# Performance work log

Measured on AMD Instinct MI355X. Metric: run time of the kernel, lower is better.

## Reference

```python
import jax, jax.numpy as jnp
import numpy as np

NSAMPLE = 32
LAMBDA = 0.5


def setup_inputs() -> dict:
    key = jax.random.key(0)
    k1, k2, k3, k4, k5 = jax.random.split(key, 5)
    B, N, NPOINT, C, NCOMP = 4, 8192, 2048, 64, 16
    xyz = jax.random.normal(k1, (B, N, 3), dtype=jnp.float32)
    new_xyz = jax.random.normal(k2, (B, NPOINT, 3), dtype=jnp.float32)
    components = jax.random.randint(k3, (B, N, 1), 0, NCOMP, dtype=jnp.int64)
    new_components = jax.random.randint(k4, (B, NPOINT, 1), 0, NCOMP, dtype=jnp.int64)
    features = jax.random.normal(k5, (B, C, N), dtype=jnp.float32)
    return {"xyz": xyz, "new_xyz": new_xyz, "components": components,
            "new_components": new_components, "features": features}


def _gag_knn(new_xyz, xyz, new_comp, comp, k, lam):
    # squared pairwise distances (B, npoint, N), same math as sum((src-dst)**2)
    diff = new_xyz[:, :, None, :] - xyz[:, None, :, :]
    dists = jnp.sum(diff * diff, axis=-1)
    # component-aware rescale
    mask = comp[:, None, :] == new_comp[:, :, None]  # (B, npoint, N)
    dists = jnp.where(mask, dists * lam, dists * (1.0 - lam))
    # full argsort then take first k (faithful to original)
    idx = jnp.argsort(dists, axis=-1)[:, :, :k]  # (B, npoint, k)
    return idx.astype(jnp.int32)


def reference(xyz, new_xyz, components, new_components, features):
    comp = components[..., 0]
    new_comp = new_components[..., 0]
    idx = _gag_knn(new_xyz, xyz, new_comp, comp, NSAMPLE, LAMBDA)  # (B, npoint, ns)

    # group xyz: gather along N -> (B, npoint, ns, 3)
    grouped_xyz = jnp.take_along_axis(xyz[:, None, :, :], idx[..., None], axis=2)
    grouped_xyz = grouped_xyz - new_xyz[:, :, None, :]
    grouped_xyz = jnp.transpose(grouped_xyz, (0, 3, 1, 2))  # (B, 3, npoint, ns)

    # group features: (B, C, N) -> (B, npoint, ns, C) -> (B, C, npoint, ns)
    feats_bnc = jnp.transpose(features, (0, 2, 1))  # (B, N, C)
    grouped_feats = jnp.take_along_axis(feats_bnc[:, None, :, :], idx[..., None], axis=2)
    grouped_feats = jnp.transpose(grouped_feats, (0, 3, 1, 2))  # (B, C, npoint, ns)

    return jnp.concatenate([grouped_xyz, grouped_feats], axis=1)  # (B, 3+C, npoint, ns)
```

## Files before the change

### kernel.cpp

```cpp
#include <hip/hip_runtime.h>


#define BQ 4
#define NN_ 8192
#define NPOINT 2048
#define CF 64
#define NS 32
#define T1 256
#define PER (NN_ / T1)
#define CAP 1024

__global__ __launch_bounds__(256) void knn_kernel(const float* __restrict__ xyz,
                                                  const float* __restrict__ new_xyz,
                                                  int* __restrict__ idxOut) {
  const int q = blockIdx.x;
  const int b = q / NPOINT;
  const int tid = threadIdx.x;

  const float qx = new_xyz[q * 3 + 0];
  const float qy = new_xyz[q * 3 + 1];
  const float qz = new_xyz[q * 3 + 2];

  const float* __restrict__ base = xyz + (size_t)b * NN_ * 3;

  float d[PER];
  float lmin = 3.4e38f;
  int n = tid;
#pragma unroll
  for (int j = 0; j < PER; j++, n += T1) {
    float dx = base[n * 3 + 0] - qx;
    float dy = base[n * 3 + 1] - qy;
    float dz = base[n * 3 + 2] - qz;
    float dist = __fadd_rn(__fadd_rn(__fmul_rn(dx, dx), __fmul_rn(dy, dy)),
                           __fmul_rn(dz, dz));
    dist *= 0.5f;
    d[j] = dist;
    lmin = fminf(lmin, dist);
  }

  __shared__ float mins[T1];
  mins[tid] = lmin;
  __syncthreads();
  for (int k = 2; k <= T1; k <<= 1) {
    for (int j = k >> 1; j > 0; j >>= 1) {
      int ixj = tid ^ j;
      if (ixj > tid) {
        float a = mins[tid], bb = mins[ixj];
        bool up = ((tid & k) == 0);
        if (up ? (a > bb) : (a < bb)) { mins[tid] = bb; mins[ixj] = a; }
      }
      __syncthreads();
    }
  }
  const float theta = mins[NS - 1];

  __shared__ unsigned long long cand[CAP];
  __shared__ int cnt;
  if (tid == 0) cnt = 0;
  __syncthreads();
  n = tid;
#pragma unroll
  for (int j = 0; j < PER; j++, n += T1) {
    if (d[j] <= theta) {
      int pos = atomicAdd(&cnt, 1);
      if (pos < CAP)
        cand[pos] = ((unsigned long long)__float_as_uint(d[j]) << 32) | (unsigned)n;
    }
  }
  __syncthreads();
  int m = cnt < CAP ? cnt : CAP;

  for (int i = tid; i < m; i += T1) {
    unsigned long long x = cand[i];
    int r = 0;
    for (int j = 0; j < m; j++) r += (cand[j] < x) ? 1 : 0;
    if (r < NS) idxOut[q * NS + r] = (int)(x & 0xffffffffu);
  }
}

__global__ __launch_bounds__(256) void transpose_kernel(const float* __restrict__ f,
                                                        float* __restrict__ ft) {
  __shared__ float t[32][33];
  const int b = blockIdx.z;
  const int n0 = blockIdx.x * 32;
  const int c0 = blockIdx.y * 32;
  const int tx = threadIdx.x;
  const int ty = threadIdx.y;
#pragma unroll
  for (int i = 0; i < 4; i++) {
    int c = c0 + ty + i * 8;
    t[ty + i * 8][tx] = f[(size_t)b * CF * NN_ + (size_t)c * NN_ + n0 + tx];
  }
  __syncthreads();
#pragma unroll
  for (int i = 0; i < 4; i++) {
    int nrow = n0 + ty + i * 8;
    ft[(size_t)b * NN_ * CF + (size_t)nrow * CF + c0 + tx] = t[tx][ty + i * 8];
  }
}

#define FSTR 68
__global__ __launch_bounds__(256) void group_kernel(const float* __restrict__ xyz,
                                                    const float* __restrict__ new_xyz,
                                                    const float* __restrict__ featsT,
                                                    const int* __restrict__ idxArr,
                                                    float* __restrict__ out) {
  const int q = blockIdx.x;
  const int b = q / NPOINT;
  const int p = q - b * NPOINT;
  const int tid = threadIdx.x;

  __shared__ int sIdx[NS];
  __shared__ __align__(16) float ldsF[NS * FSTR];
  __shared__ float ldsX[3 * NS];

  if (tid < NS) sIdx[tid] = idxArr[q * NS + tid];
  __syncthreads();

  {
    int s = tid >> 3, r = tid & 7;
    int nn = sIdx[s];
    const float4* src = (const float4*)(featsT + ((size_t)b * NN_ + nn) * CF);
    float4 v0 = src[r * 2];
    float4 v1 = src[r * 2 + 1];
    float4* dst = (float4*)(ldsF + s * FSTR + r * 8);
    dst[0] = v0;
    dst[1] = v1;
  }
  if (tid < 96) {
    int dd = tid >> 5, s = tid & 31;
    int nn = sIdx[s];
    ldsX[dd * NS + s] = xyz[((size_t)b * NN_ + nn) * 3 + dd] -
                        new_xyz[(size_t)q * 3 + dd];
  }
  __syncthreads();

  const int s = tid & 31;
  const int r0 = tid >> 5;
#pragma unroll
  for (int k = 0; k < 9; k++) {
    int row = r0 + k * 8;
    if (row < 67) {
      float v = (row < 3) ? ldsX[row * NS + s] : ldsF[s * FSTR + (row - 3)];
      out[(((size_t)b * 67 + row) * NPOINT + p) * NS + s] = v;
    }
  }
}

extern "C" void kernel_launch(void* const* d_in, const int* in_sizes, int n_in,
                              void* d_out, int out_size, void* d_ws, size_t ws_size,
                              hipStream_t stream) {
  const float* xyz      = (const float*)d_in[0];
  const float* new_xyz  = (const float*)d_in[1];
  const float* features = (const float*)d_in[4];
  float* out = (float*)d_out;

  int* idxArr = (int*)d_ws;
  float* featsT = (float*)((char*)d_ws + (size_t)BQ * NPOINT * NS * sizeof(int));

  knn_kernel<<<BQ * NPOINT, T1, 0, stream>>>(xyz, new_xyz, idxArr);
  transpose_kernel<<<dim3(NN_ / 32, CF / 32, BQ), dim3(32, 8), 0, stream>>>(features, featsT);
  group_kernel<<<BQ * NPOINT, T1, 0, stream>>>(xyz, new_xyz, featsT, idxArr, out);
}
```

Before: 156.2 us.

## Batch eight queries per block with LDS-staged points and warp-level threshold

The KNN kernel now gives each block eight queries, with one 32-lane group per query. Point coordinates are staged in LDS in chunks so all eight queries reuse each load. The 256-thread bitonic sort with many barriers is replaced by a shuffle max-of-lane-minima threshold, which is looser but still guaranteed to keep at least 32 candidates. Distances are recomputed in a second pass from global memory rather than kept in registers. The rank-based selection runs per group over a smaller candidate buffer. The cost is extra recomputation, a larger candidate set and a risk of overflowing the 768-entry buffer.

```diff
diff --git a/kernel.cpp b/kernel.cpp
--- a/kernel.cpp
+++ b/kernel.cpp
@@ -6,75 +6,93 @@
 #define NPOINT 2048
 #define CF 64
 #define NS 32
-#define T1 256
-#define PER (NN_ / T1)
-#define CAP 1024
+#define QB 8
+#define CHUNK 2048
+#define CAP 768
 
-__global__ __launch_bounds__(256) void knn_kernel(const float* __restrict__ xyz,
-                                                  const float* __restrict__ new_xyz,
-                                                  int* __restrict__ idxOut) {
-  const int q = blockIdx.x;
+__global__ __launch_bounds__(256, 3) void knn_kernel(const float* __restrict__ xyz,
+                                                     const float* __restrict__ new_xyz,
+                                                     int* __restrict__ idxOut) {
+  const int tid = threadIdx.x;
+  const int g = tid >> 5;
+  const int s = tid & 31;
+  const int q = blockIdx.x * QB + g;
   const int b = q / NPOINT;
-  const int tid = threadIdx.x;
+
+  __shared__ union {
+    float stage[CHUNK * 3];
+    unsigned long long cand[QB][CAP];
+  } sh;
+  __shared__ int cnt[QB];
 
   const float qx = new_xyz[q * 3 + 0];
   const float qy = new_xyz[q * 3 + 1];
   const float qz = new_xyz[q * 3 + 2];
-
   const float* __restrict__ base = xyz + (size_t)b * NN_ * 3;
 
-  float d[PER];
   float lmin = 3.4e38f;
-  int n = tid;
+  for (int c0 = 0; c0 < NN_; c0 += CHUNK) {
+    __syncthreads();
+    {
+      const float4* src = (const float4*)(base + (size_t)c0 * 3);
+      float4* dst = (float4*)sh.stage;
 #pragma unroll
-  for (int j = 0; j < PER; j++, n += T1) {
-    float dx = base[n * 3 + 0] - qx;
-    float dy = base[n * 3 + 1] - qy;
-    float dz = base[n * 3 + 2] - qz;
+      for (int k = 0; k < (CHUNK * 3 / 4) / 256; k++)
+        dst[tid + k * 256] = src[tid + k * 256];
+    }
+    __syncthreads();
+#pragma unroll 8
+    for (int j = 0; j < CHUNK / 32; j++) {
+      int p = s + j * 32;
+      float dx = sh.stage[p * 3 + 0] - qx;
+      float dy = sh.stage[p * 3 + 1] - qy;
+      float dz = sh.stage[p * 3 + 2] - qz;
+      float dist = __fadd_rn(__fadd_rn(__fmul_rn(dx, dx), __fmul_rn(dy, dy)),
+                             __fmul_rn(dz, dz));
+      dist *= 0.5f;
+      lmin = fminf(lmin, dist);
+    }
+  }
+
+  float th = lmin;
+#pragma unroll
+  for (int mask = 16; mask >= 1; mask >>= 1)
+    th = fmaxf(th, __shfl_xor(th, mask));
+
+  __syncthreads();
+  if (tid < QB) cnt[tid] = 0;
+  __syncthreads();
+
+#pragma unroll 4
+  for (int j = 0; j < NN_ / 32; j++) {
+    int p = s + j * 32;
+    float dx = base[p * 3 + 0] - qx;
+    float dy = base[p * 3 + 1] - qy;
+    float dz = base[p * 3 + 2] - qz;
     float dist = __fadd_rn(__fadd_rn(__fmul_rn(dx, dx), __fmul_rn(dy, dy)),
                            __fmul_rn(dz, dz));
     dist *= 0.5f;
-    d[j] = dist;
-    lmin = fminf(lmin, dist);
-  }
-
-  __shared__ float mins[T1];
-  mins[tid] = lmin;
-  __syncthreads();
-  for (int k = 2; k <= T1; k <<= 1) {
-    for (int j = k >> 1; j > 0; j >>= 1) {
-      int ixj = tid ^ j;
-      if (ixj > tid) {
-        float a = mins[tid], bb = mins[ixj];
-        bool up = ((tid & k) == 0);
-        if (up ? (a > bb) : (a < bb)) { mins[tid] = bb; mins[ixj] = a; }
-      }
-      __syncthreads();
-    }
-  }
-  const float theta = mins[NS - 1];
-
-  __shared__ unsigned long long cand[CAP];
-  __shared__ int cnt;
-  if (tid == 0) cnt = 0;
-  __syncthreads();
-  n = tid;
-#pragma unroll
-  for (int j = 0; j < PER; j++, n += T1) {
-    if (d[j] <= theta) {
-      int pos = atomicAdd(&cnt, 1);
+    if (dist <= th) {
+      int pos = atomicAdd(&cnt[g], 1);
       if (pos < CAP)
-        cand[pos] = ((unsigned long long)__float_as_uint(d[j]) << 32) | (unsigned)n;
+        sh.cand[g][pos] =
+            ((unsigned long long)__float_as_uint(dist) << 32) | (unsigned)p;
     }
   }
   __syncthreads();
-  int m = cnt < CAP ? cnt : CAP;
+  const int m = cnt[g] < CAP ? cnt[g] : CAP;
 
-  for (int i = tid; i < m; i += T1) {
-    unsigned long long x = cand[i];
-    int r = 0;
-    for (int j = 0; j < m; j++) r += (cand[j] < x) ? 1 : 0;
-    if (r < NS) idxOut[q * NS + r] = (int)(x & 0xffffffffu);
+  for (int b0 = 0; b0 < m; b0 += 64) {
+    unsigned long long x0 = (b0 + s < m) ? sh.cand[g][b0 + s] : ~0ull;
+    unsigned long long x1 = (b0 + 32 + s < m) ? sh.cand[g][b0 + 32 + s] : ~0ull;
+    int r0 = 0, r1 = 0;
+    for (int j = 0; j < m; j++) {
+      unsigned long long cj = sh.cand[g][j];
+      r0 += (cj < x0) ? 1 : 0;
+      r1 += (cj < x1) ? 1 : 0;
+    }
+    if (b0 + s < m && r0 < NS) idxOut[(size_t)q * NS + r0] = (int)(unsigned)x0;
+    if (b0 + 32 + s < m && r1 < NS) idxOut[(size_t)q * NS + r1] = (int)(unsigned)x1;
   }
 }
 
@@ -158,7 +176,7 @@
   int* idxArr = (int*)d_ws;
   float* featsT = (float*)((char*)d_ws + (size_t)BQ * NPOINT * NS * sizeof(int));
 
-  knn_kernel<<<BQ * NPOINT, T1, 0, stream>>>(xyz, new_xyz, idxArr);
+  knn_kernel<<<(BQ * NPOINT) / QB, 256, 0, stream>>>(xyz, new_xyz, idxArr);
   transpose_kernel<<<dim3(NN_ / 32, CF / 32, BQ), dim3(32, 8), 0, stream>>>(features, featsT);
-  group_kernel<<<BQ * NPOINT, T1, 0, stream>>>(xyz, new_xyz, featsT, idxArr, out);
+  group_kernel<<<BQ * NPOINT, 256, 0, stream>>>(xyz, new_xyz, featsT, idxArr, out);
 }
```

Measured after the change: 288.1 us. 1.84x slower.

## Vectorize xyz loads and replace LDS bitonic threshold sort with wave shuffles

Applied to the files above, without the earlier changes.

The kNN kernel now reads xyz as float4 triples, so each thread handles four consecutive points and deinterleaves their coordinates in registers. The 256-element shared-memory bitonic sort, which needed many block barriers, is replaced by a 64-lane shuffle bitonic sort within each wave. Each wave takes its own 32nd-smallest thread minimum as the candidate threshold; that value is still an upper bound on the true 32nd-nearest distance, but it is looser and may admit more candidates. The candidate buffer is halved to 512 entries and an occupancy hint is added to launch bounds, which raises the risk of overflow if too many candidates pass the threshold.

```diff
diff --git a/kernel.cpp b/kernel.cpp
--- a/kernel.cpp
+++ b/kernel.cpp
@@ -6,75 +6,84 @@
 #define NPOINT 2048
 #define CF 64
 #define NS 32
-#define T1 256
-#define PER (NN_ / T1)
-#define CAP 1024
+#define CAP 512
 
-__global__ __launch_bounds__(256) void knn_kernel(const float* __restrict__ xyz,
-                                                  const float* __restrict__ new_xyz,
-                                                  int* __restrict__ idxOut) {
+__global__ __launch_bounds__(256, 3) void knn_kernel(const float* __restrict__ xyz,
+                                                     const float* __restrict__ new_xyz,
+                                                     int* __restrict__ idxOut) {
   const int q = blockIdx.x;
-  const int b = q / NPOINT;
+  const int b = q >> 11;
   const int tid = threadIdx.x;
 
   const float qx = new_xyz[q * 3 + 0];
   const float qy = new_xyz[q * 3 + 1];
   const float qz = new_xyz[q * 3 + 2];
 
-  const float* __restrict__ base = xyz + (size_t)b * NN_ * 3;
+  const float4* __restrict__ X4 = (const float4*)(xyz + (size_t)b * NN_ * 3);
 
-  float d[PER];
+  float d[32];
   float lmin = 3.4e38f;
-  int n = tid;
 #pragma unroll
-  for (int j = 0; j < PER; j++, n += T1) {
-    float dx = base[n * 3 + 0] - qx;
-    float dy = base[n * 3 + 1] - qy;
-    float dz = base[n * 3 + 2] - qz;
-    float dist = __fadd_rn(__fadd_rn(__fmul_rn(dx, dx), __fmul_rn(dy, dy)),
-                           __fmul_rn(dz, dz));
-    dist *= 0.5f;
-    d[j] = dist;
-    lmin = fminf(lmin, dist);
+  for (int jc = 0; jc < 8; jc++) {
+    float4 a0 = X4[3 * tid + 768 * jc + 0];
+    float4 a1 = X4[3 * tid + 768 * jc + 1];
+    float4 a2 = X4[3 * tid + 768 * jc + 2];
+    float px[4] = {a0.x, a0.w, a1.z, a2.y};
+    float py[4] = {a0.y, a1.x, a1.w, a2.z};
+    float pz[4] = {a0.z, a1.y, a2.x, a2.w};
+#pragma unroll
+    for (int i = 0; i < 4; i++) {
+      float dx = px[i] - qx;
+      float dy = py[i] - qy;
+      float dz = pz[i] - qz;
+      float dist = __fadd_rn(__fadd_rn(__fmul_rn(dx, dx), __fmul_rn(dy, dy)),
+                             __fmul_rn(dz, dz));
+      dist *= 0.5f;
+      d[jc * 4 + i] = dist;
+      lmin = fminf(lmin, dist);
+    }
   }
 
-  __shared__ float mins[T1];
-  mins[tid] = lmin;
-  __syncthreads();
-  for (int k = 2; k <= T1; k <<= 1) {
-    for (int j = k >> 1; j > 0; j >>= 1) {
-      int ixj = tid ^ j;
-      if (ixj > tid) {
-        float a = mins[tid], bb = mins[ixj];
-        bool up = ((tid & k) == 0);
-        if (up ? (a > bb) : (a < bb)) { mins[tid] = bb; mins[ixj] = a; }
+  {
+    const int lane = tid & 63;
+    float v = lmin;
+#pragma unroll
+    for (int k = 2; k <= 64; k <<= 1) {
+#pragma unroll
+      for (int j = k >> 1; j > 0; j >>= 1) {
+        float o = __shfl_xor(v, j);
+        bool dirUp = ((lane & k) == 0);
+        bool lower = ((lane & j) == 0);
+        float mn = fminf(v, o), mx = fmaxf(v, o);
+        v = (dirUp == lower) ? mn : mx;
       }
-      __syncthreads();
     }
+    lmin = __shfl(v, 31);
   }
-  const float theta = mins[NS - 1];
+  const float theta = lmin;
 
   __shared__ unsigned long long cand[CAP];
   __shared__ int cnt;
   if (tid == 0) cnt = 0;
   __syncthreads();
-  n = tid;
+
 #pragma unroll
-  for (int j = 0; j < PER; j++, n += T1) {
+  for (int j = 0; j < 32; j++) {
     if (d[j] <= theta) {
+      int n = 4 * tid + 1024 * (j >> 2) + (j & 3);
       int pos = atomicAdd(&cnt, 1);
       if (pos < CAP)
         cand[pos] = ((unsigned long long)__float_as_uint(d[j]) << 32) | (unsigned)n;
     }
   }
   __syncthreads();
-  int m = cnt < CAP ? cnt : CAP;
+  const int m = cnt < CAP ? cnt : CAP;
 
-  for (int i = tid; i < m; i += T1) {
+  for (int i = tid; i < m; i += 256) {
     unsigned long long x = cand[i];
     int r = 0;
     for (int j = 0; j < m; j++) r += (cand[j] < x) ? 1 : 0;
-    if (r < NS) idxOut[q * NS + r] = (int)(x & 0xffffffffu);
+    if (r < NS) idxOut[(size_t)q * NS + r] = (int)(unsigned)(x & 0xffffffffu);
   }
 }
 
@@ -158,7 +167,7 @@
   int* idxArr = (int*)d_ws;
   float* featsT = (float*)((char*)d_ws + (size_t)BQ * NPOINT * NS * sizeof(int));
 
-  knn_kernel<<<BQ * NPOINT, T1, 0, stream>>>(xyz, new_xyz, idxArr);
+  knn_kernel<<<BQ * NPOINT, 256, 0, stream>>>(xyz, new_xyz, idxArr);
   transpose_kernel<<<dim3(NN_ / 32, CF / 32, BQ), dim3(32, 8), 0, stream>>>(features, featsT);
-  group_kernel<<<BQ * NPOINT, T1, 0, stream>>>(xyz, new_xyz, featsT, idxArr, out);
+  group_kernel<<<BQ * NPOINT, 256, 0, stream>>>(xyz, new_xyz, featsT, idxArr, out);
 }
```

Measured after the change: 175.4 us. 1.12x slower.
